# Kernel optimization log

Hardware: AMD Instinct MI355X
Metric: run time of the kernel (lower is better)

## Reference

```python
import jax, jax.numpy as jnp
import numpy as np

I_SIZE = (256, 256)   # (H, W)
C_FACTOR = 2.0
CPOINT = 160
BATCH = 8
CH = 2                # channels of alpha (2D displacement field)
BIG = 1e10


def _grid_xy():
    # torch: meshgrid('ij') of linspace per dim, stack at dim2, then [:, :, [1, 0]] -> (x, y)
    H, W = I_SIZE
    yy, xx = jnp.meshgrid(jnp.arange(H, dtype=jnp.float32),
                          jnp.arange(W, dtype=jnp.float32), indexing='ij')
    return jnp.stack([xx, yy], axis=-1)  # [H, W, 2] = (x, y)


def _support_radius(cpoint_loc):
    # MaxMinPointDist: per batch, max over points of min distance to other points.
    # Use squared distances to keep sqrt away from the zero diagonal.
    diff = cpoint_loc[:, :, None, :] - cpoint_loc[:, None, :, :]   # [B, N, N, 2]
    sq = jnp.sum(diff * diff, axis=-1)                             # [B, N, N]
    N = cpoint_loc.shape[1]
    sq = sq + jnp.eye(N, dtype=sq.dtype) * BIG                     # mask self-distance
    return jnp.sqrt(jnp.max(jnp.min(sq, axis=2), axis=1))          # [B]


def setup_inputs() -> dict:
    key = jax.random.key(0)
    k1, k2 = jax.random.split(key)
    H, W = I_SIZE
    scale = jnp.array([W - 1.0, H - 1.0], dtype=jnp.float32)
    cpoint_loc = jax.random.uniform(k1, (BATCH, CPOINT, 2), dtype=jnp.float32) * scale
    alpha = jax.random.normal(k2, (BATCH, CPOINT, CH), dtype=jnp.float32)
    return {"cpoint_loc": cpoint_loc, "alpha": alpha}


def reference(cpoint_loc, alpha):
    # cpoint_loc: [B, N, 2], alpha: [B, N, C]
    c = _support_radius(cpoint_loc) * C_FACTOR                 # [B]
    loc = _grid_xy()                                           # [H, W, 2]
    diff = loc[None, :, :, None, :] - cpoint_loc[:, None, None, :, :]  # [B, H, W, N, 2]
    dist = jnp.linalg.norm(diff, axis=-1) / c[:, None, None, None]     # [B, H, W, N]
    # Wendland C2 kernel with compact support dist < 1
    weight = jnp.where(dist < 1.0,
                       jnp.power(1.0 - dist, 4) * (4.0 * dist + 1.0),
                       0.0)                                    # [B, H, W, N]
    phi = jnp.einsum('bhwn,bnc->bchw', weight, alpha)          # fused sum over N
    return phi


if __name__ == '__main__':
    out = reference(**setup_inputs())
    print(out.shape)
```

## Files before the change

### kernel.cpp

```cpp
#include <hip/hip_runtime.h>

#define HGT 256
#define WID 256
#define NPT 160
#define NBATCH 8
#define RPB 4

__global__ __launch_bounds__(256) void rbf_fused_kernel(const float* __restrict__ cpoint,
                                                        const float* __restrict__ alpha,
                                                        float* __restrict__ out) {
    const int tid = threadIdx.x;
    const int lane = tid & 63;
    const int wv = tid >> 6;
    const int b = blockIdx.x >> 6;
    const int blk = blockIdx.x & 63;
    const int h0 = blk * RPB;

    __shared__ float2 spts[NPT];
    __shared__ float sred[256];
    __shared__ float s_invc;
    __shared__ float4 wl[4][NPT + 4];

    const float2* cp2 = reinterpret_cast<const float2*>(cpoint) + b * NPT;
    const float2* al2 = reinterpret_cast<const float2*>(alpha) + b * NPT;

    if (tid < NPT) spts[tid] = cp2[tid];
    __syncthreads();

    float m = 0.0f;
    if (tid < NPT) {
        float minv = 1e10f;
        const float2 pi = spts[tid];
#pragma unroll 8
        for (int j = 0; j < NPT; ++j) {
            float dx = pi.x - spts[j].x;
            float dy = pi.y - spts[j].y;
            float s = fmaf(dy, dy, dx * dx);
            s = (j == tid) ? 1e10f : s;
            minv = fminf(minv, s);
        }
        m = minv;
    }
    sred[tid] = m;
    __syncthreads();
    for (int s = 128; s > 0; s >>= 1) {
        if (tid < s) sred[tid] = fmaxf(sred[tid], sred[tid + s]);
        __syncthreads();
    }
    if (tid == 0) s_invc = 1.0f / (2.0f * sqrtf(sred[0]));
    __syncthreads();
    const float inv_c = s_invc;

    const float wx0 = (float)(wv * 64) * inv_c;
    const float wx1 = (float)(wv * 64 + 63) * inv_c;
    const float wy0 = (float)h0 * inv_c;
    const float wy1 = (float)(h0 + RPB - 1) * inv_c;

    int cnt = 0;
    for (int r = 0; r < 3; ++r) {
        const int n = r * 64 + lane;
        bool keep = false;
        float4 q;
        if (n < NPT) {
            float2 p = spts[n];
            float2 a = al2[n];
            q = make_float4(p.x * inv_c, p.y * inv_c, a.x, a.y);
            float dxc = fmaxf(fmaxf(wx0 - q.x, q.x - wx1), 0.0f);
            float dyc = fmaxf(fmaxf(wy0 - q.y, q.y - wy1), 0.0f);
            keep = fmaf(dxc, dxc, dyc * dyc) < 1.0f;
        }
        const unsigned long long mk = __ballot(keep);
        if (keep) {
            int pre = __popcll(mk & ((1ULL << lane) - 1ULL));
            wl[wv][cnt + pre] = q;
        }
        cnt += __popcll(mk);
    }
    const int padded = (cnt + 3) & ~3;
    if (lane < padded - cnt) wl[wv][cnt + lane] = make_float4(1e9f, 1e9f, 0.0f, 0.0f);

    const float xs = (float)tid * inv_c;
    float acc0[RPB], acc1[RPB], ys[RPB];
#pragma unroll
    for (int k = 0; k < RPB; ++k) {
        acc0[k] = 0.0f;
        acc1[k] = 0.0f;
        ys[k] = (float)(h0 + k) * inv_c;
    }

    const float4* wlp = wl[wv];
#define BODY(q)                                                   \
    {                                                             \
        float dx = xs - (q).x;                                    \
        float dx2 = dx * dx;                                      \
        _Pragma("unroll")                                         \
        for (int k = 0; k < RPB; ++k) {                           \
            float dy = ys[k] - (q).y;                             \
            float d2 = fmaf(dy, dy, dx2);                         \
            float d = __builtin_amdgcn_sqrtf(d2);                 \
            float t = fmaxf(1.0f - d, 0.0f);                      \
            float g = fmaf(4.0f, d, 1.0f);                        \
            float t2 = t * t;                                     \
            float wgt = (t2 * t2) * g;                            \
            acc0[k] = fmaf(wgt, (q).z, acc0[k]);                  \
            acc1[k] = fmaf(wgt, (q).w, acc1[k]);                  \
        }                                                         \
    }

    for (int i = 0; i < padded; i += 4) {
        float4 q0 = wlp[i + 0];
        float4 q1 = wlp[i + 1];
        float4 q2 = wlp[i + 2];
        float4 q3 = wlp[i + 3];
        BODY(q0);
        BODY(q1);
        BODY(q2);
        BODY(q3);
    }
#undef BODY

#pragma unroll
    for (int k = 0; k < RPB; ++k) {
        const int h = h0 + k;
        out[((b * 2 + 0) * HGT + h) * WID + tid] = acc0[k];
        out[((b * 2 + 1) * HGT + h) * WID + tid] = acc1[k];
    }
}

extern "C" void kernel_launch(void* const* d_in, const int* in_sizes, int n_in,
                              void* d_out, int out_size, void* d_ws, size_t ws_size,
                              hipStream_t stream) {
    const float* cpoint = (const float*)d_in[0];
    const float* alpha  = (const float*)d_in[1];
    float* out = (float*)d_out;

    rbf_fused_kernel<<<NBATCH * (HGT / RPB), 256, 0, stream>>>(cpoint, alpha, out);
}
```

Before: 28.79 us.

## Split radius prep into separate kernel and cull points via readlane iteration

Moves the per-batch support-radius and point scaling into a small prep kernel that writes scaled points and inv_c to workspace, so each eval block no longer redoes the O(N^2) min-distance search. The eval kernel loads the points into registers, culls them with ballots, and iterates the surviving lanes with readlane broadcasts instead of compacting into LDS. The block reduction is also changed to wave shuffles. The cost is a second kernel launch with a dependency between the two launches, and a serialized scalar loop over the ballot masks.

```diff
diff --git a/kernel.cpp b/kernel.cpp
--- a/kernel.cpp
+++ b/kernel.cpp
@@ -6,20 +6,16 @@
 #define NBATCH 8
 #define RPB 4
 
-__global__ __launch_bounds__(256) void rbf_fused_kernel(const float* __restrict__ cpoint,
-                                                        const float* __restrict__ alpha,
-                                                        float* __restrict__ out) {
+
+__global__ __launch_bounds__(256) void rbf_prep_kernel(const float* __restrict__ cpoint,
+                                                       const float* __restrict__ alpha,
+                                                       float4* __restrict__ pd,
+                                                       float* __restrict__ invc) {
+    const int b = blockIdx.x;
     const int tid = threadIdx.x;
-    const int lane = tid & 63;
-    const int wv = tid >> 6;
-    const int b = blockIdx.x >> 6;
-    const int blk = blockIdx.x & 63;
-    const int h0 = blk * RPB;
-
     __shared__ float2 spts[NPT];
-    __shared__ float sred[256];
+    __shared__ float sred[4];
     __shared__ float s_invc;
-    __shared__ float4 wl[4][NPT + 4];
 
     const float2* cp2 = reinterpret_cast<const float2*>(cpoint) + b * NPT;
     const float2* al2 = reinterpret_cast<const float2*>(alpha) + b * NPT;
@@ -41,43 +37,61 @@
         }
         m = minv;
     }
-    sred[tid] = m;
+#pragma unroll
+    for (int off = 32; off > 0; off >>= 1) m = fmaxf(m, __shfl_xor(m, off));
+    if ((tid & 63) == 0) sred[tid >> 6] = m;
     __syncthreads();
-    for (int s = 128; s > 0; s >>= 1) {
-        if (tid < s) sred[tid] = fmaxf(sred[tid], sred[tid + s]);
-        __syncthreads();
+    if (tid == 0) {
+        float mm = fmaxf(fmaxf(sred[0], sred[1]), fmaxf(sred[2], sred[3]));
+        s_invc = 1.0f / (2.0f * sqrtf(mm));
+        invc[b] = s_invc;
     }
-    if (tid == 0) s_invc = 1.0f / (2.0f * sqrtf(sred[0]));
     __syncthreads();
-    const float inv_c = s_invc;
+    const float ic = s_invc;
+    if (tid < NPT) {
+        float2 p = spts[tid];
+        float2 a = al2[tid];
+        pd[b * NPT + tid] = make_float4(p.x * ic, p.y * ic, a.x, a.y);
+    }
+}
+
+__device__ __forceinline__ float rdlane(float v, int l) {
+    return __int_as_float(__builtin_amdgcn_readlane(__float_as_int(v), l));
+}
+
+__global__ __launch_bounds__(256) void rbf_eval_kernel(const float4* __restrict__ pd,
+                                                       const float* __restrict__ invc,
+                                                       float* __restrict__ out) {
+    const int tid = threadIdx.x;
+    const int lane = tid & 63;
+    const int wv = tid >> 6;
+    const int b = blockIdx.x >> 6;
+    const int blk = blockIdx.x & 63;
+    const int h0 = blk * RPB;
+
+    const float inv_c = invc[b];
+    const float4* base = pd + b * NPT;
+
+    float4 q0 = base[lane];
+    float4 q1 = base[64 + lane];
+    const int n2 = 128 + lane;
+    const bool v2 = (n2 < NPT);
+    float4 q2 = base[v2 ? n2 : 0];
 
     const float wx0 = (float)(wv * 64) * inv_c;
     const float wx1 = (float)(wv * 64 + 63) * inv_c;
     const float wy0 = (float)h0 * inv_c;
     const float wy1 = (float)(h0 + RPB - 1) * inv_c;
 
-    int cnt = 0;
-    for (int r = 0; r < 3; ++r) {
-        const int n = r * 64 + lane;
-        bool keep = false;
-        float4 q;
-        if (n < NPT) {
-            float2 p = spts[n];
-            float2 a = al2[n];
-            q = make_float4(p.x * inv_c, p.y * inv_c, a.x, a.y);
-            float dxc = fmaxf(fmaxf(wx0 - q.x, q.x - wx1), 0.0f);
-            float dyc = fmaxf(fmaxf(wy0 - q.y, q.y - wy1), 0.0f);
-            keep = fmaf(dxc, dxc, dyc * dyc) < 1.0f;
-        }
-        const unsigned long long mk = __ballot(keep);
-        if (keep) {
-            int pre = __popcll(mk & ((1ULL << lane) - 1ULL));
-            wl[wv][cnt + pre] = q;
-        }
-        cnt += __popcll(mk);
-    }
-    const int padded = (cnt + 3) & ~3;
-    if (lane < padded - cnt) wl[wv][cnt + lane] = make_float4(1e9f, 1e9f, 0.0f, 0.0f);
+#define CULL(q) (fmaf(fmaxf(fmaxf(wx0 - (q).x, (q).x - wx1), 0.0f),              \
+                      fmaxf(fmaxf(wx0 - (q).x, (q).x - wx1), 0.0f),              \
+                      fmaxf(fmaxf(wy0 - (q).y, (q).y - wy1), 0.0f) *             \
+                      fmaxf(fmaxf(wy0 - (q).y, (q).y - wy1), 0.0f)) < 1.0f)
+
+    unsigned long long m0 = __ballot(CULL(q0));
+    unsigned long long m1 = __ballot(CULL(q1));
+    unsigned long long m2 = __ballot(v2 && CULL(q2));
+#undef CULL
 
     const float xs = (float)tid * inv_c;
     float acc0[RPB], acc1[RPB], ys[RPB];
@@ -88,36 +102,32 @@
         ys[k] = (float)(h0 + k) * inv_c;
     }
 
-    const float4* wlp = wl[wv];
-#define BODY(q)                                                   \
+#define SBODY(q)                                                  \
     {                                                             \
-        float dx = xs - (q).x;                                    \
+        const float px = rdlane((q).x, l);                        \
+        const float py = rdlane((q).y, l);                        \
+        const float pa = rdlane((q).z, l);                        \
+        const float pb = rdlane((q).w, l);                        \
+        float dx = xs - px;                                       \
         float dx2 = dx * dx;                                      \
         _Pragma("unroll")                                         \
         for (int k = 0; k < RPB; ++k) {                           \
-            float dy = ys[k] - (q).y;                             \
+            float dy = ys[k] - py;                                \
             float d2 = fmaf(dy, dy, dx2);                         \
             float d = __builtin_amdgcn_sqrtf(d2);                 \
             float t = fmaxf(1.0f - d, 0.0f);                      \
             float g = fmaf(4.0f, d, 1.0f);                        \
             float t2 = t * t;                                     \
             float wgt = (t2 * t2) * g;                            \
-            acc0[k] = fmaf(wgt, (q).z, acc0[k]);                  \
-            acc1[k] = fmaf(wgt, (q).w, acc1[k]);                  \
+            acc0[k] = fmaf(wgt, pa, acc0[k]);                     \
+            acc1[k] = fmaf(wgt, pb, acc1[k]);                     \
         }                                                         \
     }
 
-    for (int i = 0; i < padded; i += 4) {
-        float4 q0 = wlp[i + 0];
-        float4 q1 = wlp[i + 1];
-        float4 q2 = wlp[i + 2];
-        float4 q3 = wlp[i + 3];
-        BODY(q0);
-        BODY(q1);
-        BODY(q2);
-        BODY(q3);
-    }
-#undef BODY
+    while (m0) { const int l = __builtin_ctzll(m0); m0 &= (m0 - 1); SBODY(q0); }
+    while (m1) { const int l = __builtin_ctzll(m1); m1 &= (m1 - 1); SBODY(q1); }
+    while (m2) { const int l = __builtin_ctzll(m2); m2 &= (m2 - 1); SBODY(q2); }
+#undef SBODY
 
 #pragma unroll
     for (int k = 0; k < RPB; ++k) {
@@ -132,7 +142,10 @@
                               hipStream_t stream) {
     const float* cpoint = (const float*)d_in[0];
     const float* alpha  = (const float*)d_in[1];
-    float* out = (float*)d_out;
+    float4* pd  = (float4*)d_ws;
+    float* invc = (float*)((char*)d_ws + NBATCH * NPT * sizeof(float4));
+    float* out  = (float*)d_out;
 
-    rbf_fused_kernel<<<NBATCH * (HGT / RPB), 256, 0, stream>>>(cpoint, alpha, out);
+    rbf_prep_kernel<<<NBATCH, 256, 0, stream>>>(cpoint, alpha, pd, invc);
+    rbf_eval_kernel<<<NBATCH * (HGT / RPB), 256, 0, stream>>>(pd, invc, out);
 }
```

Result: slower. 31.04 us (+7.8%).

## Split support-radius prep into separate kernel and halve rows per block

Applied to the files above, without the earlier changes.

Moves the per-batch O(N^2) min-distance and support-radius computation out of every eval block into a small prep kernel. The prep kernel writes scaled point/alpha float4 records and inv_c to workspace, so the redundant per-block radius computation goes away. Rows per block drop from 4 to 2, doubling the grid to 1024 blocks for more parallelism. The prep reduction now uses wave shuffles instead of a shared-memory tree. The cost is a second kernel launch with a serial dependency, plus less reuse of each culled point list across rows.

```diff
diff --git a/kernel.cpp b/kernel.cpp
--- a/kernel.cpp
+++ b/kernel.cpp
@@ -4,22 +4,18 @@
 #define WID 256
 #define NPT 160
 #define NBATCH 8
-#define RPB 4
+#define RPB 2
 
-__global__ __launch_bounds__(256) void rbf_fused_kernel(const float* __restrict__ cpoint,
-                                                        const float* __restrict__ alpha,
-                                                        float* __restrict__ out) {
+
+__global__ __launch_bounds__(256) void rbf_prep_kernel(const float* __restrict__ cpoint,
+                                                       const float* __restrict__ alpha,
+                                                       float4* __restrict__ pd,
+                                                       float* __restrict__ invc) {
+    const int b = blockIdx.x;
     const int tid = threadIdx.x;
-    const int lane = tid & 63;
-    const int wv = tid >> 6;
-    const int b = blockIdx.x >> 6;
-    const int blk = blockIdx.x & 63;
-    const int h0 = blk * RPB;
-
     __shared__ float2 spts[NPT];
-    __shared__ float sred[256];
+    __shared__ float sred[4];
     __shared__ float s_invc;
-    __shared__ float4 wl[4][NPT + 4];
 
     const float2* cp2 = reinterpret_cast<const float2*>(cpoint) + b * NPT;
     const float2* al2 = reinterpret_cast<const float2*>(alpha) + b * NPT;
@@ -41,15 +37,38 @@
         }
         m = minv;
     }
-    sred[tid] = m;
+#pragma unroll
+    for (int off = 32; off > 0; off >>= 1) m = fmaxf(m, __shfl_xor(m, off));
+    if ((tid & 63) == 0) sred[tid >> 6] = m;
     __syncthreads();
-    for (int s = 128; s > 0; s >>= 1) {
-        if (tid < s) sred[tid] = fmaxf(sred[tid], sred[tid + s]);
-        __syncthreads();
+    if (tid == 0) {
+        float mm = fmaxf(fmaxf(sred[0], sred[1]), fmaxf(sred[2], sred[3]));
+        s_invc = 1.0f / (2.0f * sqrtf(mm));
+        invc[b] = s_invc;
     }
-    if (tid == 0) s_invc = 1.0f / (2.0f * sqrtf(sred[0]));
     __syncthreads();
-    const float inv_c = s_invc;
+    const float ic = s_invc;
+    if (tid < NPT) {
+        float2 p = spts[tid];
+        float2 a = al2[tid];
+        pd[b * NPT + tid] = make_float4(p.x * ic, p.y * ic, a.x, a.y);
+    }
+}
+
+__global__ __launch_bounds__(256) void rbf_eval_kernel(const float4* __restrict__ pd,
+                                                       const float* __restrict__ invc,
+                                                       float* __restrict__ out) {
+    const int tid = threadIdx.x;
+    const int lane = tid & 63;
+    const int wv = tid >> 6;
+    const int b = blockIdx.x >> 7;
+    const int blk = blockIdx.x & 127;
+    const int h0 = blk * RPB;
+
+    __shared__ float4 wl[4][NPT + 4];
+
+    const float inv_c = invc[b];
+    const float4* base = pd + b * NPT;
 
     const float wx0 = (float)(wv * 64) * inv_c;
     const float wx1 = (float)(wv * 64 + 63) * inv_c;
@@ -57,14 +76,13 @@
     const float wy1 = (float)(h0 + RPB - 1) * inv_c;
 
     int cnt = 0;
+#pragma unroll
     for (int r = 0; r < 3; ++r) {
         const int n = r * 64 + lane;
         bool keep = false;
         float4 q;
         if (n < NPT) {
-            float2 p = spts[n];
-            float2 a = al2[n];
-            q = make_float4(p.x * inv_c, p.y * inv_c, a.x, a.y);
+            q = base[n];
             float dxc = fmaxf(fmaxf(wx0 - q.x, q.x - wx1), 0.0f);
             float dyc = fmaxf(fmaxf(wy0 - q.y, q.y - wy1), 0.0f);
             keep = fmaf(dxc, dxc, dyc * dyc) < 1.0f;
@@ -132,7 +150,10 @@
                               hipStream_t stream) {
     const float* cpoint = (const float*)d_in[0];
     const float* alpha  = (const float*)d_in[1];
-    float* out = (float*)d_out;
+    float4* pd  = (float4*)d_ws;
+    float* invc = (float*)((char*)d_ws + NBATCH * NPT * sizeof(float4));
+    float* out  = (float*)d_out;
 
-    rbf_fused_kernel<<<NBATCH * (HGT / RPB), 256, 0, stream>>>(cpoint, alpha, out);
+    rbf_prep_kernel<<<NBATCH, 256, 0, stream>>>(cpoint, alpha, pd, invc);
+    rbf_eval_kernel<<<NBATCH * (HGT / RPB), 256, 0, stream>>>(pd, invc, out);
 }
```

Result: faster. 27.71 us (-3.7%).
